# Performance work log

Hardware: AMD Instinct MI355X
Metric: run time of the kernel (lower is better)

Reference implementation:

```python
import jax, jax.numpy as jnp
import numpy as np

HEAD_DIM = 32
KERNEL = 3
DILATION = 2


def _unfold(x, k, dil):
    """torch.nn.Unfold with stride=1, padding=dil*(k-1)//2.
    x: [B, C, H, W] -> patches [B, C, k*k, H, W] (kernel positions row-major,
    channel-major overall, matching torch's (B, C*k*k, L) layout)."""
    B, C, H, W = x.shape
    pad = dil * (k - 1) // 2
    xp = jnp.pad(x, ((0, 0), (0, 0), (pad, pad), (pad, pad)))
    patches = jnp.stack(
        [xp[:, :, i * dil:i * dil + H, j * dil:j * dil + W]
         for i in range(k) for j in range(k)],
        axis=2,
    )
    return patches  # [B, C, k*k, H, W]


def setup_inputs() -> dict:
    key = jax.random.key(0)
    kq, kk, kv = jax.random.split(key, 3)
    shape = (8, 384, 56, 56)
    return {
        "q": jax.random.normal(kq, shape, dtype=jnp.float32),
        "k": jax.random.normal(kk, shape, dtype=jnp.float32),
        "v": jax.random.normal(kv, shape, dtype=jnp.float32),
    }


def reference(q, k, v):
    B, d, H, W = q.shape
    h = d // HEAD_DIM
    N = H * W
    k2 = KERNEL * KERNEL
    scale = HEAD_DIM ** (-0.5)

    # q: [B, h, N, hd]
    qr = q.reshape(B, h, HEAD_DIM, N).transpose(0, 1, 3, 2)
    # k patches: [B, h, hd, k2, N]
    kp = _unfold(k, KERNEL, DILATION).reshape(B, h, HEAD_DIM, k2, N)
    attn = jnp.einsum('bhnd,bhdkn->bhnk', qr, kp) * scale
    attn = jax.nn.softmax(attn, axis=-1)
    # v patches: [B, h, hd, k2, N]
    vp = _unfold(v, KERNEL, DILATION).reshape(B, h, HEAD_DIM, k2, N)
    out = jnp.einsum('bhnk,bhdkn->bhnd', attn, vp)  # [B, h, N, hd]
    # transpose(1,2) then reshape(B, H, W, d)
    return out.transpose(0, 2, 1, 3).reshape(B, H, W, d)
```

## Files before the change

kernel.cpp:

```cpp
#include <hip/hip_runtime.h>

#define HD 32
#define HALF 16
#define NHEADS 12
#define HH 56
#define WW 56
#define NN (HH * WW)
#define BB 8
#define CC (HD * NHEADS)
#define TILE_N 128
#define SCALE 0.17677669529663689f

__global__ __launch_bounds__(256) void dilate_attn_kernel(
    const float* __restrict__ q,
    const float* __restrict__ k,
    const float* __restrict__ v,
    float* __restrict__ out)
{
    const int xi = threadIdx.x;
    const int half = threadIdx.y;
    const int n = blockIdx.x * TILE_N + xi;
    const int bh = blockIdx.y;
    const int b = bh / NHEADS;
    const int head = bh - b * NHEADS;
    const bool active = (n < NN);

    const int y = n / WW;
    const int x = n - y * WW;

    const size_t base = ((size_t)b * CC + (size_t)head * HD + (size_t)half * HALF) * NN;

    __shared__ float part[2][TILE_N][9];

    float qv[HALF];
    if (active) {
        const float* qb = q + base + n;
#pragma unroll
        for (int d = 0; d < HALF; ++d) qv[d] = qb[(size_t)d * NN];
    }

    float lg[9];
#pragma unroll
    for (int t = 0; t < 9; ++t) {
        const int dy = ((t / 3) - 1) * 2;
        const int dx = ((t % 3) - 1) * 2;
        const int ny = y + dy;
        const int nx = x + dx;
        float s = 0.f;
        if (active && (unsigned)ny < HH && (unsigned)nx < WW) {
            const float* kb = k + base + (size_t)(ny * WW + nx);
#pragma unroll
            for (int d = 0; d < HALF; ++d) s = fmaf(qv[d], kb[(size_t)d * NN], s);
        }
        lg[t] = s;
        part[half][xi][t] = s;
    }
    __syncthreads();

    {
        const int other = 1 - half;
#pragma unroll
        for (int t = 0; t < 9; ++t)
            lg[t] = (lg[t] + part[other][xi][t]) * SCALE;
    }
    float m = lg[0];
#pragma unroll
    for (int t = 1; t < 9; ++t) m = fmaxf(m, lg[t]);
    float wsum = 0.f;
#pragma unroll
    for (int t = 0; t < 9; ++t) { lg[t] = __expf(lg[t] - m); wsum += lg[t]; }
    const float inv = 1.f / wsum;

    float acc[HALF];
#pragma unroll
    for (int d = 0; d < HALF; ++d) acc[d] = 0.f;
#pragma unroll
    for (int t = 0; t < 9; ++t) {
        const int dy = ((t / 3) - 1) * 2;
        const int dx = ((t % 3) - 1) * 2;
        const int ny = y + dy;
        const int nx = x + dx;
        if (active && (unsigned)ny < HH && (unsigned)nx < WW) {
            const float w = lg[t] * inv;
            const float* vb = v + base + (size_t)(ny * WW + nx);
#pragma unroll
            for (int d = 0; d < HALF; ++d) acc[d] = fmaf(w, vb[(size_t)d * NN], acc[d]);
        }
    }

    if (active) {
        float* ob = out + (((size_t)b * HH + y) * WW + x) * CC
                    + (size_t)head * HD + (size_t)half * HALF;
#pragma unroll
        for (int d = 0; d < HALF; d += 4) {
            float4 val = make_float4(acc[d], acc[d + 1], acc[d + 2], acc[d + 3]);
            *reinterpret_cast<float4*>(ob + d) = val;
        }
    }
}

extern "C" void kernel_launch(void* const* d_in, const int* in_sizes, int n_in,
                              void* d_out, int out_size, void* d_ws, size_t ws_size,
                              hipStream_t stream) {
    const float* q = (const float*)d_in[0];
    const float* k = (const float*)d_in[1];
    const float* v = (const float*)d_in[2];
    float* out = (float*)d_out;

    dim3 block(TILE_N, 2);
    dim3 grid((NN + TILE_N - 1) / TILE_N, BB * NHEADS);
    dilate_attn_kernel<<<grid, block, 0, stream>>>(q, k, v, out);
}
```

Baseline: 185.2 us.

## Process four pixels per thread with vectorized window loads and 4-way channel split

```diff
diff --git a/kernel.cpp b/kernel.cpp
--- a/kernel.cpp
+++ b/kernel.cpp
@@ -1,100 +1,166 @@
 #include <hip/hip_runtime.h>
 
 #define HD 32
-#define HALF 16
 #define NHEADS 12
 #define HH 56
 #define WW 56
 #define NN (HH * WW)
 #define BB 8
 #define CC (HD * NHEADS)
-#define TILE_N 128
+#define TOTAL (BB * CC * NN)
+#define QCH 8
+#define CHUNKS 32
+#define TILE_N (CHUNKS * 4)
 #define SCALE 0.17677669529663689f
 
-__global__ __launch_bounds__(256) void dilate_attn_kernel(
+__global__ __launch_bounds__(128, 3) void dilate_attn_kernel(
     const float* __restrict__ q,
     const float* __restrict__ k,
     const float* __restrict__ v,
     float* __restrict__ out)
 {
-    const int xi = threadIdx.x;
-    const int half = threadIdx.y;
-    const int n = blockIdx.x * TILE_N + xi;
+    const int tx = threadIdx.x;
+    const int qy = threadIdx.y;
+    const int n0 = blockIdx.x * TILE_N + tx * 4;
     const int bh = blockIdx.y;
     const int b = bh / NHEADS;
     const int head = bh - b * NHEADS;
-    const bool active = (n < NN);
+    const bool active = (n0 < NN);
 
-    const int y = n / WW;
-    const int x = n - y * WW;
+    const int y = n0 / WW;
+    const int x0 = n0 - y * WW;
+    const bool xlo = (x0 == 0);
+    const bool xhi = (x0 == WW - 4);
 
-    const size_t base = ((size_t)b * CC + (size_t)head * HD + (size_t)half * HALF) * NN;
+    const int base0 = (b * CC + head * HD + qy * QCH) * NN;
 
-    __shared__ float part[2][TILE_N][9];
+    __shared__ float4 part[4][CHUNKS][9];
 
-    float qv[HALF];
+    float qv[QCH][4];
     if (active) {
-        const float* qb = q + base + n;
 #pragma unroll
-        for (int d = 0; d < HALF; ++d) qv[d] = qb[(size_t)d * NN];
+        for (int d = 0; d < QCH; ++d) {
+            const float4 t = *reinterpret_cast<const float4*>(q + base0 + d * NN + n0);
+            qv[d][0] = t.x; qv[d][1] = t.y; qv[d][2] = t.z; qv[d][3] = t.w;
+        }
+    } else {
+#pragma unroll
+        for (int d = 0; d < QCH; ++d)
+#pragma unroll
+            for (int j = 0; j < 4; ++j) qv[d][j] = 0.f;
     }
 
-    float lg[9];
+    float lg[9][4];
 #pragma unroll
-    for (int t = 0; t < 9; ++t) {
-        const int dy = ((t / 3) - 1) * 2;
-        const int dx = ((t % 3) - 1) * 2;
-        const int ny = y + dy;
-        const int nx = x + dx;
+    for (int t = 0; t < 9; ++t)
+#pragma unroll
+        for (int j = 0; j < 4; ++j) lg[t][j] = 0.f;
+
+#pragma unroll
+    for (int r = 0; r < 3; ++r) {
+        const int ny = y + (r - 1) * 2;
+        const bool rv = active && ((unsigned)ny < HH);
+#pragma unroll
+        for (int d = 0; d < QCH; ++d) {
+            float w[8];
+            if (rv) {
+                const int si = base0 + d * NN + ny * WW + x0;
+                int silo = si - 2;            if (silo < 0) silo = 0;
+                int sihi = si + 4;            if (sihi > TOTAL - 2) sihi = TOTAL - 2;
+                const float2 lo  = *reinterpret_cast<const float2*>(k + silo);
+                const float4 mid = *reinterpret_cast<const float4*>(k + si);
+                const float2 hi  = *reinterpret_cast<const float2*>(k + sihi);
+                w[0] = lo.x; w[1] = lo.y;
+                w[2] = mid.x; w[3] = mid.y; w[4] = mid.z; w[5] = mid.w;
+                w[6] = hi.x; w[7] = hi.y;
+                if (xlo) { w[0] = 0.f; w[1] = 0.f; }
+                if (xhi) { w[6] = 0.f; w[7] = 0.f; }
+            } else {
+#pragma unroll
+                for (int e = 0; e < 8; ++e) w[e] = 0.f;
+            }
+#pragma unroll
+            for (int dx = 0; dx < 3; ++dx)
+#pragma unroll
+                for (int j = 0; j < 4; ++j)
+                    lg[r * 3 + dx][j] = fmaf(qv[d][j], w[dx * 2 + j], lg[r * 3 + dx][j]);
+        }
+    }
+
+#pragma unroll
+    for (int t = 0; t < 9; ++t)
+        part[qy][tx][t] = make_float4(lg[t][0], lg[t][1], lg[t][2], lg[t][3]);
+    __syncthreads();
+#pragma unroll
+    for (int qq = 1; qq < 4; ++qq) {
+        const int oq = (qy + qq) & 3;
+#pragma unroll
+        for (int t = 0; t < 9; ++t) {
+            const float4 p = part[oq][tx][t];
+            lg[t][0] += p.x; lg[t][1] += p.y; lg[t][2] += p.z; lg[t][3] += p.w;
+        }
+    }
+
+#pragma unroll
+    for (int t = 0; t < 9; ++t)
+#pragma unroll
+        for (int j = 0; j < 4; ++j) lg[t][j] *= SCALE;
+#pragma unroll
+    for (int j = 0; j < 4; ++j) {
+        float m = lg[0][j];
+#pragma unroll
+        for (int t = 1; t < 9; ++t) m = fmaxf(m, lg[t][j]);
         float s = 0.f;
-        if (active && (unsigned)ny < HH && (unsigned)nx < WW) {
-            const float* kb = k + base + (size_t)(ny * WW + nx);
 #pragma unroll
-            for (int d = 0; d < HALF; ++d) s = fmaf(qv[d], kb[(size_t)d * NN], s);
-        }
-        lg[t] = s;
-        part[half][xi][t] = s;
+        for (int t = 0; t < 9; ++t) { const float e = __expf(lg[t][j] - m); lg[t][j] = e; s += e; }
+        const float inv = 1.f / s;
+#pragma unroll
+        for (int t = 0; t < 9; ++t) lg[t][j] *= inv;
     }
-    __syncthreads();
 
-    {
-        const int other = 1 - half;
+    float acc[QCH][4];
 #pragma unroll
-        for (int t = 0; t < 9; ++t)
-            lg[t] = (lg[t] + part[other][xi][t]) * SCALE;
-    }
-    float m = lg[0];
+    for (int d = 0; d < QCH; ++d)
 #pragma unroll
-    for (int t = 1; t < 9; ++t) m = fmaxf(m, lg[t]);
-    float wsum = 0.f;
+        for (int j = 0; j < 4; ++j) acc[d][j] = 0.f;
+
 #pragma unroll
-    for (int t = 0; t < 9; ++t) { lg[t] = __expf(lg[t] - m); wsum += lg[t]; }
-    const float inv = 1.f / wsum;
-
-    float acc[HALF];
+    for (int r = 0; r < 3; ++r) {
+        const int ny = y + (r - 1) * 2;
+        const bool rv = active && ((unsigned)ny < HH);
 #pragma unroll
-    for (int d = 0; d < HALF; ++d) acc[d] = 0.f;
+        for (int d = 0; d < QCH; ++d) {
+            float w[8];
+            if (rv) {
+                const int si = base0 + d * NN + ny * WW + x0;
+                int silo = si - 2;            if (silo < 0) silo = 0;
+                int sihi = si + 4;            if (sihi > TOTAL - 2) sihi = TOTAL - 2;
+                const float2 lo  = *reinterpret_cast<const float2*>(v + silo);
+                const float4 mid = *reinterpret_cast<const float4*>(v + si);
+                const float2 hi  = *reinterpret_cast<const float2*>(v + sihi);
+                w[0] = lo.x; w[1] = lo.y;
+                w[2] = mid.x; w[3] = mid.y; w[4] = mid.z; w[5] = mid.w;
+                w[6] = hi.x; w[7] = hi.y;
+                if (xlo) { w[0] = 0.f; w[1] = 0.f; }
+                if (xhi) { w[6] = 0.f; w[7] = 0.f; }
+            } else {
 #pragma unroll
-    for (int t = 0; t < 9; ++t) {
-        const int dy = ((t / 3) - 1) * 2;
-        const int dx = ((t % 3) - 1) * 2;
-        const int ny = y + dy;
-        const int nx = x + dx;
-        if (active && (unsigned)ny < HH && (unsigned)nx < WW) {
-            const float w = lg[t] * inv;
-            const float* vb = v + base + (size_t)(ny * WW + nx);
+                for (int e = 0; e < 8; ++e) w[e] = 0.f;
+            }
 #pragma unroll
-            for (int d = 0; d < HALF; ++d) acc[d] = fmaf(w, vb[(size_t)d * NN], acc[d]);
+            for (int dx = 0; dx < 3; ++dx)
+#pragma unroll
+                for (int j = 0; j < 4; ++j)
+                    acc[d][j] = fmaf(lg[r * 3 + dx][j], w[dx * 2 + j], acc[d][j]);
         }
     }
 
     if (active) {
-        float* ob = out + (((size_t)b * HH + y) * WW + x) * CC
-                    + (size_t)head * HD + (size_t)half * HALF;
 #pragma unroll
-        for (int d = 0; d < HALF; d += 4) {
-            float4 val = make_float4(acc[d], acc[d + 1], acc[d + 2], acc[d + 3]);
-            *reinterpret_cast<float4*>(ob + d) = val;
+        for (int j = 0; j < 4; ++j) {
+            float* ob = out + ((b * HH + y) * WW + (x0 + j)) * CC + head * HD + qy * QCH;
+            *reinterpret_cast<float4*>(ob)     = make_float4(acc[0][j], acc[1][j], acc[2][j], acc[3][j]);
+            *reinterpret_cast<float4*>(ob + 4) = make_float4(acc[4][j], acc[5][j], acc[6][j], acc[7][j]);
         }
     }
 }
@@ -107,7 +173,7 @@
     const float* v = (const float*)d_in[2];
     float* out = (float*)d_out;
 
-    dim3 block(TILE_N, 2);
+    dim3 block(CHUNKS, 4);
     dim3 grid((NN + TILE_N - 1) / TILE_N, BB * NHEADS);
     dilate_attn_kernel<<<grid, block, 0, stream>>>(q, k, v, out);
 }
```

Result: slower. 362.2 us (+95.5%).

## Stage K/V row tiles in swizzled LDS per image row and split head dim four ways

Applied to the files above, without the earlier changes.

```diff
diff --git a/kernel.cpp b/kernel.cpp
--- a/kernel.cpp
+++ b/kernel.cpp
@@ -1,15 +1,40 @@
 #include <hip/hip_runtime.h>
 
 #define HD 32
-#define HALF 16
 #define NHEADS 12
 #define HH 56
 #define WW 56
 #define NN (HH * WW)
 #define BB 8
 #define CC (HD * NHEADS)
-#define TILE_N 128
 #define SCALE 0.17677669529663689f
+
+__device__ __forceinline__ int lds_addr(int r, int p, int quad, int lane4) {
+    return ((r * 60 + p) << 5) + ((quad ^ (p & 7)) << 2) + lane4;
+}
+
+__device__ __forceinline__ void stage_tile(const float* __restrict__ src,
+                                           float* lds, int bhbase, int y, int tid) {
+#pragma unroll
+    for (int j = 0; j < 12; ++j) {
+        const int i = tid + j * 256;
+        if (i < 2880) {
+            const int r   = i / 960;
+            const int rem = i - r * 960;
+            const int ch  = rem / 30;
+            const int s   = rem - ch * 30;
+            const int ny  = y + (r - 1) * 2;
+            float2 val = make_float2(0.f, 0.f);
+            if ((unsigned)ny < HH && s >= 1 && s <= 28) {
+                val = *reinterpret_cast<const float2*>(
+                    src + bhbase + ch * NN + ny * WW + (2 * s - 2));
+            }
+            const int p0 = 2 * s;
+            lds[lds_addr(r, p0,     ch >> 2, ch & 3)] = val.x;
+            lds[lds_addr(r, p0 + 1, ch >> 2, ch & 3)] = val.y;
+        }
+    }
+}
 
 __global__ __launch_bounds__(256) void dilate_attn_kernel(
     const float* __restrict__ q,
@@ -17,52 +42,64 @@
     const float* __restrict__ v,
     float* __restrict__ out)
 {
-    const int xi = threadIdx.x;
-    const int half = threadIdx.y;
-    const int n = blockIdx.x * TILE_N + xi;
-    const int bh = blockIdx.y;
-    const int b = bh / NHEADS;
+    const int tid = threadIdx.x;
+    const int x   = tid & 63;
+    const int qc  = tid >> 6;
+    const int y   = blockIdx.x;
+    const int bh  = blockIdx.y;
+    const int b   = bh / NHEADS;
     const int head = bh - b * NHEADS;
-    const bool active = (n < NN);
+    const bool active = (x < WW);
+    const int xc = active ? x : (WW - 1);
 
-    const int y = n / WW;
-    const int x = n - y * WW;
+    __shared__ float lds[5760];
+    float* part = lds;
 
-    const size_t base = ((size_t)b * CC + (size_t)head * HD + (size_t)half * HALF) * NN;
+    const int bhbase = (b * CC + head * HD) * NN;
 
-    __shared__ float part[2][TILE_N][9];
+    float qv[8];
+    if (active) {
+        const float* qb = q + bhbase + (qc * 8) * NN + y * WW + x;
+#pragma unroll
+        for (int d = 0; d < 8; ++d) qv[d] = qb[d * NN];
+    } else {
+#pragma unroll
+        for (int d = 0; d < 8; ++d) qv[d] = 0.f;
+    }
 
-    float qv[HALF];
-    if (active) {
-        const float* qb = q + base + n;
-#pragma unroll
-        for (int d = 0; d < HALF; ++d) qv[d] = qb[(size_t)d * NN];
-    }
+    stage_tile(k, lds, bhbase, y, tid);
+    __syncthreads();
 
     float lg[9];
 #pragma unroll
-    for (int t = 0; t < 9; ++t) {
-        const int dy = ((t / 3) - 1) * 2;
-        const int dx = ((t % 3) - 1) * 2;
-        const int ny = y + dy;
-        const int nx = x + dx;
-        float s = 0.f;
-        if (active && (unsigned)ny < HH && (unsigned)nx < WW) {
-            const float* kb = k + base + (size_t)(ny * WW + nx);
+    for (int r = 0; r < 3; ++r) {
 #pragma unroll
-            for (int d = 0; d < HALF; ++d) s = fmaf(qv[d], kb[(size_t)d * NN], s);
+        for (int dxi = 0; dxi < 3; ++dxi) {
+            const int p = xc + 2 * dxi;
+            const float4 A = *reinterpret_cast<const float4*>(&lds[lds_addr(r, p, 2 * qc,     0)]);
+            const float4 B = *reinterpret_cast<const float4*>(&lds[lds_addr(r, p, 2 * qc + 1, 0)]);
+            float s = 0.f;
+            s = fmaf(qv[0], A.x, s); s = fmaf(qv[1], A.y, s);
+            s = fmaf(qv[2], A.z, s); s = fmaf(qv[3], A.w, s);
+            s = fmaf(qv[4], B.x, s); s = fmaf(qv[5], B.y, s);
+            s = fmaf(qv[6], B.z, s); s = fmaf(qv[7], B.w, s);
+            lg[r * 3 + dxi] = s;
         }
-        lg[t] = s;
-        part[half][xi][t] = s;
     }
     __syncthreads();
 
-    {
-        const int other = 1 - half;
 #pragma unroll
-        for (int t = 0; t < 9; ++t)
-            lg[t] = (lg[t] + part[other][xi][t]) * SCALE;
+    for (int t = 0; t < 9; ++t) part[(qc * 64 + x) * 9 + t] = lg[t];
+    __syncthreads();
+#pragma unroll
+    for (int o = 1; o < 4; ++o) {
+        const int oq = (qc + o) & 3;
+#pragma unroll
+        for (int t = 0; t < 9; ++t) lg[t] += part[(oq * 64 + x) * 9 + t];
     }
+
+#pragma unroll
+    for (int t = 0; t < 9; ++t) lg[t] *= SCALE;
     float m = lg[0];
 #pragma unroll
     for (int t = 1; t < 9; ++t) m = fmaxf(m, lg[t]);
@@ -70,32 +107,36 @@
 #pragma unroll
     for (int t = 0; t < 9; ++t) { lg[t] = __expf(lg[t] - m); wsum += lg[t]; }
     const float inv = 1.f / wsum;
+#pragma unroll
+    for (int t = 0; t < 9; ++t) lg[t] *= inv;
 
-    float acc[HALF];
+    __syncthreads();
+
+    stage_tile(v, lds, bhbase, y, tid);
+    __syncthreads();
+
+    float acc[8];
 #pragma unroll
-    for (int d = 0; d < HALF; ++d) acc[d] = 0.f;
+    for (int d = 0; d < 8; ++d) acc[d] = 0.f;
 #pragma unroll
-    for (int t = 0; t < 9; ++t) {
-        const int dy = ((t / 3) - 1) * 2;
-        const int dx = ((t % 3) - 1) * 2;
-        const int ny = y + dy;
-        const int nx = x + dx;
-        if (active && (unsigned)ny < HH && (unsigned)nx < WW) {
-            const float w = lg[t] * inv;
-            const float* vb = v + base + (size_t)(ny * WW + nx);
+    for (int r = 0; r < 3; ++r) {
 #pragma unroll
-            for (int d = 0; d < HALF; ++d) acc[d] = fmaf(w, vb[(size_t)d * NN], acc[d]);
+        for (int dxi = 0; dxi < 3; ++dxi) {
+            const int p = xc + 2 * dxi;
+            const float w = lg[r * 3 + dxi];
+            const float4 A = *reinterpret_cast<const float4*>(&lds[lds_addr(r, p, 2 * qc,     0)]);
+            const float4 B = *reinterpret_cast<const float4*>(&lds[lds_addr(r, p, 2 * qc + 1, 0)]);
+            acc[0] = fmaf(w, A.x, acc[0]); acc[1] = fmaf(w, A.y, acc[1]);
+            acc[2] = fmaf(w, A.z, acc[2]); acc[3] = fmaf(w, A.w, acc[3]);
+            acc[4] = fmaf(w, B.x, acc[4]); acc[5] = fmaf(w, B.y, acc[5]);
+            acc[6] = fmaf(w, B.z, acc[6]); acc[7] = fmaf(w, B.w, acc[7]);
         }
     }
 
     if (active) {
-        float* ob = out + (((size_t)b * HH + y) * WW + x) * CC
-                    + (size_t)head * HD + (size_t)half * HALF;
-#pragma unroll
-        for (int d = 0; d < HALF; d += 4) {
-            float4 val = make_float4(acc[d], acc[d + 1], acc[d + 2], acc[d + 3]);
-            *reinterpret_cast<float4*>(ob + d) = val;
-        }
+        float* ob = out + ((b * HH + y) * WW + x) * CC + head * HD + qc * 8;
+        *reinterpret_cast<float4*>(ob)     = make_float4(acc[0], acc[1], acc[2], acc[3]);
+        *reinterpret_cast<float4*>(ob + 4) = make_float4(acc[4], acc[5], acc[6], acc[7]);
     }
 }
 
@@ -107,7 +148,7 @@
     const float* v = (const float*)d_in[2];
     float* out = (float*)d_out;
 
-    dim3 block(TILE_N, 2);
-    dim3 grid((NN + TILE_N - 1) / TILE_N, BB * NHEADS);
+    dim3 block(256);
+    dim3 grid(HH, BB * NHEADS);
     dilate_attn_kernel<<<grid, block, 0, stream>>>(q, k, v, out);
 }
```

Result: slower. 223.2 us (+20.5%).
